# Kernel optimization log

Hardware: AMD Instinct MI355X
Metric: run time of the kernel (lower is better)

## Reference

```python
import jax, jax.numpy as jnp
import numpy as np

D = 1024      # model_dim
H = 2048      # expert hidden_dim
E = 8         # num routed experts
TOP_K = 2
N_SHARED = 1
B, S = 2, 1024


def setup_inputs() -> dict:
    key = jax.random.key(0)
    ks = jax.random.split(key, 12)
    sc = 0.02
    return {
        "hidden": jax.random.normal(ks[0], (B, S, D), jnp.float32),
        # router Linear(D -> E); stored as [in, out]
        "router_w": jax.random.normal(ks[1], (D, E), jnp.float32) * sc,
        "router_b": jnp.zeros((E,), jnp.float32),
        # shared expert (1): Linear(D->H), Linear(H->D)
        "sw1": jax.random.normal(ks[2], (D, H), jnp.float32) * sc,
        "sb1": jnp.zeros((H,), jnp.float32),
        "sw2": jax.random.normal(ks[3], (H, D), jnp.float32) * sc,
        "sb2": jnp.zeros((D,), jnp.float32),
        # routed experts, stacked over E
        "rw1": jax.random.normal(ks[4], (E, D, H), jnp.float32) * sc,
        "rb1": jnp.zeros((E, H), jnp.float32),
        "rw2": jax.random.normal(ks[5], (E, H, D), jnp.float32) * sc,
        "rb2": jnp.zeros((E, D), jnp.float32),
    }


def reference(hidden, router_w, router_b, sw1, sb1, sw2, sb2, rw1, rb1, rw2, rb2):
    b, s, d = hidden.shape
    T = b * s
    flat = hidden.reshape(T, d)                              # [T, D]

    # --- router ---
    router_logits = flat @ router_w + router_b               # [T, E]
    router_probs = jax.nn.softmax(router_logits, axis=-1)
    topk_probs, topk_idx = jax.lax.top_k(router_probs, TOP_K)  # [T, K]

    # per-(token, expert) mixing weight: sum of top-k probs that hit expert e
    weights = jnp.zeros_like(router_probs).at[
        jnp.arange(T)[:, None], topk_idx
    ].add(topk_probs)                                        # [T, E]

    # --- shared expert(s) (1 expert -> mean == itself) ---
    sh = jax.nn.gelu(flat @ sw1 + sb1, approximate=False)    # [T, H]
    shared_out = (sh @ sw2 + sb2) / N_SHARED                 # [T, D]

    # --- routed experts: dense all-expert eval weighted by routing weights ---
    # (identical math to the gather/FFN/index_add loop: weight is 0 for
    #  tokens not routed to expert e)
    h1 = jax.nn.gelu(jnp.einsum('td,edh->teh', flat, rw1) + rb1[None],
                     approximate=False)                      # [T, E, H]
    expert_out = jnp.einsum('teh,ehd->ted', h1, rw2) + rb2[None]  # [T, E, D]
    mixed = jnp.einsum('ted,te->td', expert_out, weights)    # [T, D]

    return (shared_out + mixed).reshape(b, s, d)
```

## Files before the change

kernel.cpp:

```cpp
#include <hip/hip_runtime.h>
#include <hip/hip_bf16.h>

#define T_TOK 2048
#define DDIM  1024
#define HDIM  2048
#define NEXP  8
#define NSEG  9

typedef unsigned short u16;
typedef __attribute__((ext_vector_type(4))) float f32x4;
typedef __attribute__((ext_vector_type(8))) short bf16x8;
typedef __attribute__((ext_vector_type(4))) unsigned short u16x4;

__device__ __forceinline__ u16 f2bf(float x) {
  union { float f; unsigned int u; } v; v.f = x;
  unsigned int r = v.u + 0x7fffu + ((v.u >> 16) & 1u);
  return (u16)(r >> 16);
}
__device__ __forceinline__ float gelu_exact(float x) {
  return 0.5f * x * (1.0f + erff(x * 0.70710678118654752f));
}

__device__ __forceinline__ void gload16(const void* g, void* l) {
  __builtin_amdgcn_global_load_lds(
      (const __attribute__((address_space(1))) unsigned int*)g,
      (__attribute__((address_space(3))) unsigned int*)l, 16, 0, 0);
}

__global__ __launch_bounds__(256) void router_kernel(
    const float* __restrict__ x, const float* __restrict__ rw,
    const float* __restrict__ rb, u16* __restrict__ xb,
    float* __restrict__ weights, int* __restrict__ counts,
    int* __restrict__ lists)
{
  int wv = threadIdx.x >> 6, lane = threadIdx.x & 63;
  int t = blockIdx.x * 4 + wv;
  const float* xrow = x + (size_t)t * DDIM;
  float acc[NEXP];
#pragma unroll
  for (int e = 0; e < NEXP; e++) acc[e] = 0.f;
#pragma unroll
  for (int i = 0; i < 4; i++) {
    int d0 = i * 256 + lane * 4;
    f32x4 xv = *(const f32x4*)(xrow + d0);
    u16x4 pk;
#pragma unroll
    for (int j = 0; j < 4; j++) {
      float xs = xv[j];
      pk[j] = f2bf(xs);
      const float* wr = rw + (size_t)(d0 + j) * NEXP;
#pragma unroll
      for (int e = 0; e < NEXP; e++) acc[e] = fmaf(xs, wr[e], acc[e]);
    }
    *(u16x4*)(xb + (size_t)t * DDIM + d0) = pk;
  }
#pragma unroll
  for (int off = 32; off >= 1; off >>= 1)
#pragma unroll
    for (int e = 0; e < NEXP; e++) acc[e] += __shfl_xor(acc[e], off);

  if (lane == 0) {
    float lg[NEXP], mx = -1e30f;
#pragma unroll
    for (int e = 0; e < NEXP; e++) { lg[e] = acc[e] + rb[e]; mx = fmaxf(mx, lg[e]); }
    float p[NEXP], s = 0.f;
#pragma unroll
    for (int e = 0; e < NEXP; e++) { p[e] = expf(lg[e] - mx); s += p[e]; }
    float inv = 1.0f / s;
#pragma unroll
    for (int e = 0; e < NEXP; e++) p[e] *= inv;
    int i1 = 0;
#pragma unroll
    for (int e = 1; e < NEXP; e++) if (p[e] > p[i1]) i1 = e;
    int i2 = (i1 == 0) ? 1 : 0;
#pragma unroll
    for (int e = 0; e < NEXP; e++) if (e != i1 && p[e] > p[i2]) i2 = e;
#pragma unroll
    for (int e = 0; e < NEXP; e++)
      weights[(size_t)t * NEXP + e] = (e == i1) ? p[i1] : (e == i2) ? p[i2] : 0.f;
    int p1 = atomicAdd(counts + i1, 1); lists[i1 * T_TOK + p1] = t;
    int p2 = atomicAdd(counts + i2, 1); lists[i2 * T_TOK + p2] = t;
    lists[NEXP * T_TOK + t] = t;
  }
}

__global__ void seg_kernel(int* counts, int* segoff, int* ytab, int* nyt) {
  counts[NEXP] = T_TOK;
  int off = 0, n = 0;
  for (int e = 0; e < NSEG; e++) {
    segoff[e] = off;
    int c = counts[e];
    for (int my = 0; my * 128 < c; my++) ytab[n++] = e * 256 + my;
    off += c;
  }
  *nyt = n;
}

__global__ __launch_bounds__(256) void transpose_bf16_kernel(
    const float* __restrict__ rin, const float* __restrict__ sin_,
    u16* __restrict__ rout, u16* __restrict__ sout, int R, int C)
{
  __shared__ float tile[32][33];
  int b = blockIdx.z;
  const float* inb = (b < NEXP) ? rin + (size_t)b * R * C : sin_;
  u16* outb = (b < NEXP) ? rout + (size_t)b * R * C : sout;
  int r0 = blockIdx.y * 32, c0 = blockIdx.x * 32;
  int tx = threadIdx.x & 31, ty = threadIdx.x >> 5;
#pragma unroll
  for (int j = 0; j < 4; j++) {
    int r = ty + j * 8;
    tile[r][tx] = inb[(size_t)(r0 + r) * C + c0 + tx];
  }
  __syncthreads();
#pragma unroll
  for (int j = 0; j < 4; j++) {
    int rr = ty + j * 8;
    outb[(size_t)(c0 + rr) * R + r0 + tx] = f2bf(tile[tx][rr]);
  }
}

__global__ __launch_bounds__(256) void gemm1_kernel(
    const u16* __restrict__ Xb, const u16* __restrict__ rw1t,
    const u16* __restrict__ sw1t, const float* __restrict__ rb1,
    const float* __restrict__ sb1, const int* __restrict__ counts,
    const int* __restrict__ segoff, const int* __restrict__ lists,
    const int* __restrict__ ytab, const int* __restrict__ nyt,
    u16* __restrict__ H1)
{
  __shared__ u16 Alds[128 * 64];
  __shared__ u16 Blds[128 * 64];

  int tid = threadIdx.x, wv = tid >> 6, lane = tid & 63;
  int wm = wv >> 1, wn = wv & 1;
  int col8 = (lane & 7) * 8;

  int ntile = nyt[0] * (HDIM / 128);
  for (int t = blockIdx.x; t < ntile; t += gridDim.x) {
    int yt = t >> 4, nx = t & 15;
    int em = ytab[yt];
    int e = em >> 8, m0 = (em & 255) * 128, n0 = nx * 128;
    int cnt = counts[e];
    const u16* Bt = (e < NEXP) ? (rw1t + (size_t)e * HDIM * DDIM) : sw1t;
    const float* bias = (e < NEXP) ? (rb1 + (size_t)e * HDIM) : sb1;
    const int* list = lists + e * T_TOK;
    int seg = segoff[e];

    size_t asrc[4], bsrc[4];
#pragma unroll
    for (int r = 0; r < 4; r++) {
      int srow = r * 32 + wv * 8 + (lane >> 3);
      int tok = list[min(m0 + srow, cnt - 1)];
      asrc[r] = (size_t)tok * DDIM + col8;
      bsrc[r] = (size_t)(n0 + srow) * DDIM + col8;
    }

    f32x4 acc[4][4];
#pragma unroll
    for (int i = 0; i < 4; i++)
#pragma unroll
      for (int j = 0; j < 4; j++) acc[i][j] = (f32x4){0.f, 0.f, 0.f, 0.f};

    for (int kk = 0; kk < DDIM; kk += 64) {
#pragma unroll
      for (int r = 0; r < 4; r++) {
        gload16(Xb + asrc[r] + kk, Alds + (size_t)(r * 256 + wv * 64 + lane) * 8);
        gload16(Bt + bsrc[r] + kk, Blds + (size_t)(r * 256 + wv * 64 + lane) * 8);
      }
      __syncthreads();
#pragma unroll
      for (int ks = 0; ks < 2; ks++) {
        int kb = ks * 32 + (lane >> 4) * 8;
        bf16x8 af[4], bfr[4];
#pragma unroll
        for (int f = 0; f < 4; f++) {
          af[f]  = *(const bf16x8*)(Alds + (wm * 64 + f * 16 + (lane & 15)) * 64 + kb);
          bfr[f] = *(const bf16x8*)(Blds + (wn * 64 + f * 16 + (lane & 15)) * 64 + kb);
        }
#pragma unroll
        for (int mf = 0; mf < 4; mf++)
#pragma unroll
          for (int nf = 0; nf < 4; nf++)
            acc[mf][nf] = __builtin_amdgcn_mfma_f32_16x16x32_bf16(af[mf], bfr[nf], acc[mf][nf], 0, 0, 0);
      }
      __syncthreads();
    }

#pragma unroll
    for (int nf = 0; nf < 4; nf++) {
      int col = n0 + wn * 64 + nf * 16 + (lane & 15);
      float b = bias[col];
#pragma unroll
      for (int mf = 0; mf < 4; mf++) {
#pragma unroll
        for (int rg = 0; rg < 4; rg++) {
          int mt = wm * 64 + mf * 16 + (lane >> 4) * 4 + rg;
          if (m0 + mt < cnt) {
            float v = acc[mf][nf][rg] + b;
            H1[(size_t)(seg + m0 + mt) * HDIM + col] = f2bf(gelu_exact(v));
          }
        }
      }
    }
  }
}

__global__ __launch_bounds__(256) void gemm2_kernel(
    const u16* __restrict__ H1, const u16* __restrict__ rw2t,
    const u16* __restrict__ sw2t, const float* __restrict__ rb2,
    const float* __restrict__ sb2, const float* __restrict__ weights,
    const int* __restrict__ counts, const int* __restrict__ segoff,
    const int* __restrict__ lists, const int* __restrict__ ytab,
    const int* __restrict__ nyt, float* __restrict__ out)
{
  __shared__ u16 Alds[128 * 64];
  __shared__ u16 Blds[128 * 64];

  int tid = threadIdx.x, wv = tid >> 6, lane = tid & 63;
  int wm = wv >> 1, wn = wv & 1;
  int col8 = (lane & 7) * 8;

  int ntile = nyt[0] * (DDIM / 128);
  for (int t = blockIdx.x; t < ntile; t += gridDim.x) {
    int yt = t >> 3, nx = t & 7;
    int em = ytab[yt];
    int e = em >> 8, m0 = (em & 255) * 128, n0 = nx * 128;
    int cnt = counts[e];
    const u16* Bt = (e < NEXP) ? (rw2t + (size_t)e * DDIM * HDIM) : sw2t;
    const float* bias = (e < NEXP) ? (rb2 + (size_t)e * DDIM) : sb2;
    const int* list = lists + e * T_TOK;
    int seg = segoff[e];

    size_t asrc[4], bsrc[4];
#pragma unroll
    for (int r = 0; r < 4; r++) {
      int srow = r * 32 + wv * 8 + (lane >> 3);
      asrc[r] = (size_t)(seg + min(m0 + srow, cnt - 1)) * HDIM + col8;
      bsrc[r] = (size_t)(n0 + srow) * HDIM + col8;
    }

    f32x4 acc[4][4];
#pragma unroll
    for (int i = 0; i < 4; i++)
#pragma unroll
      for (int j = 0; j < 4; j++) acc[i][j] = (f32x4){0.f, 0.f, 0.f, 0.f};

    for (int kk = 0; kk < HDIM; kk += 64) {
#pragma unroll
      for (int r = 0; r < 4; r++) {
        gload16(H1 + asrc[r] + kk, Alds + (size_t)(r * 256 + wv * 64 + lane) * 8);
        gload16(Bt + bsrc[r] + kk, Blds + (size_t)(r * 256 + wv * 64 + lane) * 8);
      }
      __syncthreads();
#pragma unroll
      for (int ks = 0; ks < 2; ks++) {
        int kb = ks * 32 + (lane >> 4) * 8;
        bf16x8 af[4], bfr[4];
#pragma unroll
        for (int f = 0; f < 4; f++) {
          af[f]  = *(const bf16x8*)(Alds + (wm * 64 + f * 16 + (lane & 15)) * 64 + kb);
          bfr[f] = *(const bf16x8*)(Blds + (wn * 64 + f * 16 + (lane & 15)) * 64 + kb);
        }
#pragma unroll
        for (int mf = 0; mf < 4; mf++)
#pragma unroll
          for (int nf = 0; nf < 4; nf++)
            acc[mf][nf] = __builtin_amdgcn_mfma_f32_16x16x32_bf16(af[mf], bfr[nf], acc[mf][nf], 0, 0, 0);
      }
      __syncthreads();
    }

    float biasv[4];
#pragma unroll
    for (int nf = 0; nf < 4; nf++) biasv[nf] = bias[n0 + wn * 64 + nf * 16 + (lane & 15)];

#pragma unroll
    for (int mf = 0; mf < 4; mf++) {
#pragma unroll
      for (int rg = 0; rg < 4; rg++) {
        int mt = wm * 64 + mf * 16 + (lane >> 4) * 4 + rg;
        int mrow = m0 + mt;
        if (mrow < cnt) {
          int tok = list[mrow];
          float w = (e < NEXP) ? weights[(size_t)tok * NEXP + e] : 1.0f;
          float* orow = out + (size_t)tok * DDIM + n0 + wn * 64 + (lane & 15);
#pragma unroll
          for (int nf = 0; nf < 4; nf++)
            atomicAdd(orow + nf * 16, w * (acc[mf][nf][rg] + biasv[nf]));
        }
      }
    }
  }
}

extern "C" void kernel_launch(void* const* d_in, const int* in_sizes, int n_in,
                              void* d_out, int out_size, void* d_ws, size_t ws_size,
                              hipStream_t stream) {
  (void)in_sizes; (void)n_in; (void)out_size; (void)ws_size;
  const float* hidden   = (const float*)d_in[0];
  const float* router_w = (const float*)d_in[1];
  const float* router_b = (const float*)d_in[2];
  const float* sw1 = (const float*)d_in[3];
  const float* sb1 = (const float*)d_in[4];
  const float* sw2 = (const float*)d_in[5];
  const float* sb2 = (const float*)d_in[6];
  const float* rw1 = (const float*)d_in[7];
  const float* rb1 = (const float*)d_in[8];
  const float* rw2 = (const float*)d_in[9];
  const float* rb2 = (const float*)d_in[10];
  float* out = (float*)d_out;

  char* ws = (char*)d_ws;
  u16* Xb      = (u16*)(ws + 0);
  u16* rw1t    = (u16*)(ws + 4194304);
  u16* rw2t    = (u16*)(ws + 37748736);
  u16* sw1t    = (u16*)(ws + 71303168);
  u16* sw2t    = (u16*)(ws + 75497472);
  u16* H1      = (u16*)(ws + 79691776);
  float* weights = (float*)(ws + 104857600);
  int* counts  = (int*)(ws + 104923136);
  int* segoff  = (int*)(ws + 104923200);
  int* lists   = (int*)(ws + 104923264);
  int* ytab    = (int*)(ws + 104996992);
  int* nyt     = (int*)(ws + 104997632);

  hipMemsetAsync(counts, 0, 64, stream);
  hipMemsetAsync(out, 0, (size_t)T_TOK * DDIM * sizeof(float), stream);

  router_kernel<<<T_TOK / 4, 256, 0, stream>>>(hidden, router_w, router_b, Xb,
                                               weights, counts, lists);
  seg_kernel<<<1, 1, 0, stream>>>(counts, segoff, ytab, nyt);

  transpose_bf16_kernel<<<dim3(HDIM / 32, DDIM / 32, NSEG), 256, 0, stream>>>(
      rw1, sw1, rw1t, sw1t, DDIM, HDIM);
  transpose_bf16_kernel<<<dim3(DDIM / 32, HDIM / 32, NSEG), 256, 0, stream>>>(
      rw2, sw2, rw2t, sw2t, HDIM, DDIM);

  gemm1_kernel<<<1024, 256, 0, stream>>>(
      Xb, rw1t, sw1t, rb1, sb1, counts, segoff, lists, ytab, nyt, H1);
  gemm2_kernel<<<1024, 256, 0, stream>>>(
      H1, rw2t, sw2t, rb2, sb2, weights, counts, segoff, lists, ytab, nyt, out);
}
```

Baseline: 256.1 us.

## Fuse fp32 weight transpose-convert into GEMM loads, split-K gemm2, fast GELU

Drops the separate transpose/bf16 conversion kernels. Each GEMM now reads the fp32 weights directly, converts them to bf16 in registers with a one-step register prefetch, and stores them into XOR-swizzled LDS to avoid bank conflicts. gemm2 splits K into two halves to get more tiles, which doubles the output atomics. The exact erf GELU is replaced with a tanh-style sigmoid approximation, which changes numerics slightly.

```diff
diff --git a/kernel.cpp b/kernel.cpp
--- a/kernel.cpp
+++ b/kernel.cpp
@@ -11,14 +11,16 @@
 typedef __attribute__((ext_vector_type(4))) float f32x4;
 typedef __attribute__((ext_vector_type(8))) short bf16x8;
 typedef __attribute__((ext_vector_type(4))) unsigned short u16x4;
+typedef __attribute__((ext_vector_type(8))) unsigned short u16x8;
 
 __device__ __forceinline__ u16 f2bf(float x) {
   union { float f; unsigned int u; } v; v.f = x;
   unsigned int r = v.u + 0x7fffu + ((v.u >> 16) & 1u);
   return (u16)(r >> 16);
 }
-__device__ __forceinline__ float gelu_exact(float x) {
-  return 0.5f * x * (1.0f + erff(x * 0.70710678118654752f));
+__device__ __forceinline__ float gelu_fast(float x) {
+  float y = x * (1.595769122f + 0.0713548162f * x * x);
+  return x / (1.0f + __expf(-y));
 }
 
 __device__ __forceinline__ void gload16(const void* g, void* l) {
@@ -96,32 +98,10 @@
   *nyt = n;
 }
 
-__global__ __launch_bounds__(256) void transpose_bf16_kernel(
-    const float* __restrict__ rin, const float* __restrict__ sin_,
-    u16* __restrict__ rout, u16* __restrict__ sout, int R, int C)
-{
-  __shared__ float tile[32][33];
-  int b = blockIdx.z;
-  const float* inb = (b < NEXP) ? rin + (size_t)b * R * C : sin_;
-  u16* outb = (b < NEXP) ? rout + (size_t)b * R * C : sout;
-  int r0 = blockIdx.y * 32, c0 = blockIdx.x * 32;
-  int tx = threadIdx.x & 31, ty = threadIdx.x >> 5;
-#pragma unroll
-  for (int j = 0; j < 4; j++) {
-    int r = ty + j * 8;
-    tile[r][tx] = inb[(size_t)(r0 + r) * C + c0 + tx];
-  }
-  __syncthreads();
-#pragma unroll
-  for (int j = 0; j < 4; j++) {
-    int rr = ty + j * 8;
-    outb[(size_t)(c0 + rr) * R + r0 + tx] = f2bf(tile[tx][rr]);
-  }
-}
 
 __global__ __launch_bounds__(256) void gemm1_kernel(
-    const u16* __restrict__ Xb, const u16* __restrict__ rw1t,
-    const u16* __restrict__ sw1t, const float* __restrict__ rb1,
+    const u16* __restrict__ Xb, const float* __restrict__ rw1,
+    const float* __restrict__ sw1, const float* __restrict__ rb1,
     const float* __restrict__ sb1, const int* __restrict__ counts,
     const int* __restrict__ segoff, const int* __restrict__ lists,
     const int* __restrict__ ytab, const int* __restrict__ nyt,
@@ -130,9 +110,27 @@
   __shared__ u16 Alds[128 * 64];
   __shared__ u16 Blds[128 * 64];
 
-  int tid = threadIdx.x, wv = tid >> 6, lane = tid & 63;
-  int wm = wv >> 1, wn = wv & 1;
-  int col8 = (lane & 7) * 8;
+  int tid = threadIdx.x, lane = tid & 63;
+  int wv = tid >> 6, wm = wv >> 1, wn = wv & 1;
+  int kc = lane >> 4, lr = lane & 15;
+
+  int srow[4]; int achk[4];
+#pragma unroll
+  for (int r = 0; r < 4; r++) {
+    srow[r] = r * 32 + wv * 8 + (lane >> 3);
+    achk[r] = ((lane & 7) ^ (srow[r] & 7)) * 8;
+  }
+  int aoff[2][4], boff[2][4];
+#pragma unroll
+  for (int ks = 0; ks < 2; ks++)
+#pragma unroll
+    for (int f = 0; f < 4; f++) {
+      int ra = wm * 64 + f * 16 + lr;
+      int rb_ = wn * 64 + f * 16 + lr;
+      aoff[ks][f] = ra * 64 + (((ks * 4 + kc) ^ (ra & 7)) * 8);
+      boff[ks][f] = rb_ * 64 + (((ks * 4 + kc) ^ (rb_ & 7)) * 8);
+    }
+  int h8 = tid >> 5, bn = (lane & 31) * 4;
 
   int ntile = nyt[0] * (HDIM / 128);
   for (int t = blockIdx.x; t < ntile; t += gridDim.x) {
@@ -140,19 +138,18 @@
     int em = ytab[yt];
     int e = em >> 8, m0 = (em & 255) * 128, n0 = nx * 128;
     int cnt = counts[e];
-    const u16* Bt = (e < NEXP) ? (rw1t + (size_t)e * HDIM * DDIM) : sw1t;
+    const float* Wf = (e < NEXP) ? (rw1 + (size_t)e * DDIM * HDIM) : sw1;
     const float* bias = (e < NEXP) ? (rb1 + (size_t)e * HDIM) : sb1;
     const int* list = lists + e * T_TOK;
     int seg = segoff[e];
 
-    size_t asrc[4], bsrc[4];
+    size_t asrc[4];
 #pragma unroll
     for (int r = 0; r < 4; r++) {
-      int srow = r * 32 + wv * 8 + (lane >> 3);
-      int tok = list[min(m0 + srow, cnt - 1)];
-      asrc[r] = (size_t)tok * DDIM + col8;
-      bsrc[r] = (size_t)(n0 + srow) * DDIM + col8;
-    }
+      int tok = list[min(m0 + srow[r], cnt - 1)];
+      asrc[r] = (size_t)tok * DDIM + achk[r];
+    }
+    const float* Wb = Wf + n0 + bn;
 
     f32x4 acc[4][4];
 #pragma unroll
@@ -160,21 +157,40 @@
 #pragma unroll
       for (int j = 0; j < 4; j++) acc[i][j] = (f32x4){0.f, 0.f, 0.f, 0.f};
 
-    for (int kk = 0; kk < DDIM; kk += 64) {
-#pragma unroll
-      for (int r = 0; r < 4; r++) {
+    f32x4 vb[8];
+    {
+      const float* Wk = Wb + (size_t)(h8 * 8) * HDIM;
+#pragma unroll
+      for (int q = 0; q < 8; q++) vb[q] = *(const f32x4*)(Wk + (size_t)q * HDIM);
+    }
+
+    const int NS = DDIM / 64;
+    for (int s = 0; s < NS; s++) {
+      int kk = s * 64;
+#pragma unroll
+      for (int r = 0; r < 4; r++)
         gload16(Xb + asrc[r] + kk, Alds + (size_t)(r * 256 + wv * 64 + lane) * 8);
-        gload16(Bt + bsrc[r] + kk, Blds + (size_t)(r * 256 + wv * 64 + lane) * 8);
+#pragma unroll
+      for (int j = 0; j < 4; j++) {
+        u16x8 pk;
+#pragma unroll
+        for (int q = 0; q < 8; q++) pk[q] = f2bf(vb[q][j]);
+        int row = bn + j;
+        *(u16x8*)(Blds + (size_t)row * 64 + ((h8 ^ (row & 7)) * 8)) = pk;
       }
       __syncthreads();
+      if (s + 1 < NS) {
+        const float* Wk = Wb + (size_t)((s + 1) * 64 + h8 * 8) * HDIM;
+#pragma unroll
+        for (int q = 0; q < 8; q++) vb[q] = *(const f32x4*)(Wk + (size_t)q * HDIM);
+      }
 #pragma unroll
       for (int ks = 0; ks < 2; ks++) {
-        int kb = ks * 32 + (lane >> 4) * 8;
         bf16x8 af[4], bfr[4];
 #pragma unroll
         for (int f = 0; f < 4; f++) {
-          af[f]  = *(const bf16x8*)(Alds + (wm * 64 + f * 16 + (lane & 15)) * 64 + kb);
-          bfr[f] = *(const bf16x8*)(Blds + (wn * 64 + f * 16 + (lane & 15)) * 64 + kb);
+          af[f]  = *(const bf16x8*)(Alds + aoff[ks][f]);
+          bfr[f] = *(const bf16x8*)(Blds + boff[ks][f]);
         }
 #pragma unroll
         for (int mf = 0; mf < 4; mf++)
@@ -187,16 +203,16 @@
 
 #pragma unroll
     for (int nf = 0; nf < 4; nf++) {
-      int col = n0 + wn * 64 + nf * 16 + (lane & 15);
+      int col = n0 + wn * 64 + nf * 16 + lr;
       float b = bias[col];
 #pragma unroll
       for (int mf = 0; mf < 4; mf++) {
 #pragma unroll
         for (int rg = 0; rg < 4; rg++) {
-          int mt = wm * 64 + mf * 16 + (lane >> 4) * 4 + rg;
+          int mt = wm * 64 + mf * 16 + kc * 4 + rg;
           if (m0 + mt < cnt) {
             float v = acc[mf][nf][rg] + b;
-            H1[(size_t)(seg + m0 + mt) * HDIM + col] = f2bf(gelu_exact(v));
+            H1[(size_t)(seg + m0 + mt) * HDIM + col] = f2bf(gelu_fast(v));
           }
         }
       }
@@ -205,8 +221,8 @@
 }
 
 __global__ __launch_bounds__(256) void gemm2_kernel(
-    const u16* __restrict__ H1, const u16* __restrict__ rw2t,
-    const u16* __restrict__ sw2t, const float* __restrict__ rb2,
+    const u16* __restrict__ H1, const float* __restrict__ rw2,
+    const float* __restrict__ sw2, const float* __restrict__ rb2,
     const float* __restrict__ sb2, const float* __restrict__ weights,
     const int* __restrict__ counts, const int* __restrict__ segoff,
     const int* __restrict__ lists, const int* __restrict__ ytab,
@@ -215,28 +231,45 @@
   __shared__ u16 Alds[128 * 64];
   __shared__ u16 Blds[128 * 64];
 
-  int tid = threadIdx.x, wv = tid >> 6, lane = tid & 63;
-  int wm = wv >> 1, wn = wv & 1;
-  int col8 = (lane & 7) * 8;
-
-  int ntile = nyt[0] * (DDIM / 128);
+  int tid = threadIdx.x, lane = tid & 63;
+  int wv = tid >> 6, wm = wv >> 1, wn = wv & 1;
+  int kc = lane >> 4, lr = lane & 15;
+
+  int srow[4]; int achk[4];
+#pragma unroll
+  for (int r = 0; r < 4; r++) {
+    srow[r] = r * 32 + wv * 8 + (lane >> 3);
+    achk[r] = ((lane & 7) ^ (srow[r] & 7)) * 8;
+  }
+  int aoff[2][4], boff[2][4];
+#pragma unroll
+  for (int ks = 0; ks < 2; ks++)
+#pragma unroll
+    for (int f = 0; f < 4; f++) {
+      int ra = wm * 64 + f * 16 + lr;
+      int rb_ = wn * 64 + f * 16 + lr;
+      aoff[ks][f] = ra * 64 + (((ks * 4 + kc) ^ (ra & 7)) * 8);
+      boff[ks][f] = rb_ * 64 + (((ks * 4 + kc) ^ (rb_ & 7)) * 8);
+    }
+  int h8 = tid >> 5, bn = (lane & 31) * 4;
+
+  int ntile = nyt[0] * (DDIM / 128) * 2;
   for (int t = blockIdx.x; t < ntile; t += gridDim.x) {
-    int yt = t >> 3, nx = t & 7;
+    int kh = t & 1, nx = (t >> 1) & 7, yt = t >> 4;
     int em = ytab[yt];
     int e = em >> 8, m0 = (em & 255) * 128, n0 = nx * 128;
     int cnt = counts[e];
-    const u16* Bt = (e < NEXP) ? (rw2t + (size_t)e * DDIM * HDIM) : sw2t;
+    const float* Wf = (e < NEXP) ? (rw2 + (size_t)e * HDIM * DDIM) : sw2;
     const float* bias = (e < NEXP) ? (rb2 + (size_t)e * DDIM) : sb2;
     const int* list = lists + e * T_TOK;
     int seg = segoff[e];
-
-    size_t asrc[4], bsrc[4];
-#pragma unroll
-    for (int r = 0; r < 4; r++) {
-      int srow = r * 32 + wv * 8 + (lane >> 3);
-      asrc[r] = (size_t)(seg + min(m0 + srow, cnt - 1)) * HDIM + col8;
-      bsrc[r] = (size_t)(n0 + srow) * HDIM + col8;
-    }
+    int k0 = kh * 1024;
+
+    size_t asrc[4];
+#pragma unroll
+    for (int r = 0; r < 4; r++)
+      asrc[r] = (size_t)(seg + min(m0 + srow[r], cnt - 1)) * HDIM + k0 + achk[r];
+    const float* Wb = Wf + (size_t)k0 * DDIM + n0 + bn;
 
     f32x4 acc[4][4];
 #pragma unroll
@@ -244,21 +277,40 @@
 #pragma unroll
       for (int j = 0; j < 4; j++) acc[i][j] = (f32x4){0.f, 0.f, 0.f, 0.f};
 
-    for (int kk = 0; kk < HDIM; kk += 64) {
-#pragma unroll
-      for (int r = 0; r < 4; r++) {
+    f32x4 vb[8];
+    {
+      const float* Wk = Wb + (size_t)(h8 * 8) * DDIM;
+#pragma unroll
+      for (int q = 0; q < 8; q++) vb[q] = *(const f32x4*)(Wk + (size_t)q * DDIM);
+    }
+
+    const int NS = 1024 / 64;
+    for (int s = 0; s < NS; s++) {
+      int kk = s * 64;
+#pragma unroll
+      for (int r = 0; r < 4; r++)
         gload16(H1 + asrc[r] + kk, Alds + (size_t)(r * 256 + wv * 64 + lane) * 8);
-        gload16(Bt + bsrc[r] + kk, Blds + (size_t)(r * 256 + wv * 64 + lane) * 8);
+#pragma unroll
+      for (int j = 0; j < 4; j++) {
+        u16x8 pk;
+#pragma unroll
+        for (int q = 0; q < 8; q++) pk[q] = f2bf(vb[q][j]);
+        int row = bn + j;
+        *(u16x8*)(Blds + (size_t)row * 64 + ((h8 ^ (row & 7)) * 8)) = pk;
       }
       __syncthreads();
+      if (s + 1 < NS) {
+        const float* Wk = Wb + (size_t)((s + 1) * 64 + h8 * 8) * DDIM;
+#pragma unroll
+        for (int q = 0; q < 8; q++) vb[q] = *(const f32x4*)(Wk + (size_t)q * DDIM);
+      }
 #pragma unroll
       for (int ks = 0; ks < 2; ks++) {
-        int kb = ks * 32 + (lane >> 4) * 8;
         bf16x8 af[4], bfr[4];
 #pragma unroll
         for (int f = 0; f < 4; f++) {
-          af[f]  = *(const bf16x8*)(Alds + (wm * 64 + f * 16 + (lane & 15)) * 64 + kb);
-          bfr[f] = *(const bf16x8*)(Blds + (wn * 64 + f * 16 + (lane & 15)) * 64 + kb);
+          af[f]  = *(const bf16x8*)(Alds + aoff[ks][f]);
+          bfr[f] = *(const bf16x8*)(Blds + boff[ks][f]);
         }
 #pragma unroll
         for (int mf = 0; mf < 4; mf++)
@@ -271,18 +323,19 @@
 
     float biasv[4];
 #pragma unroll
-    for (int nf = 0; nf < 4; nf++) biasv[nf] = bias[n0 + wn * 64 + nf * 16 + (lane & 15)];
+    for (int nf = 0; nf < 4; nf++)
+      biasv[nf] = (kh == 0) ? bias[n0 + wn * 64 + nf * 16 + lr] : 0.f;
 
 #pragma unroll
     for (int mf = 0; mf < 4; mf++) {
 #pragma unroll
       for (int rg = 0; rg < 4; rg++) {
-        int mt = wm * 64 + mf * 16 + (lane >> 4) * 4 + rg;
+        int mt = wm * 64 + mf * 16 + kc * 4 + rg;
         int mrow = m0 + mt;
         if (mrow < cnt) {
           int tok = list[mrow];
           float w = (e < NEXP) ? weights[(size_t)tok * NEXP + e] : 1.0f;
-          float* orow = out + (size_t)tok * DDIM + n0 + wn * 64 + (lane & 15);
+          float* orow = out + (size_t)tok * DDIM + n0 + wn * 64 + lr;
 #pragma unroll
           for (int nf = 0; nf < 4; nf++)
             atomicAdd(orow + nf * 16, w * (acc[mf][nf][rg] + biasv[nf]));
@@ -311,17 +364,13 @@
 
   char* ws = (char*)d_ws;
   u16* Xb      = (u16*)(ws + 0);
-  u16* rw1t    = (u16*)(ws + 4194304);
-  u16* rw2t    = (u16*)(ws + 37748736);
-  u16* sw1t    = (u16*)(ws + 71303168);
-  u16* sw2t    = (u16*)(ws + 75497472);
-  u16* H1      = (u16*)(ws + 79691776);
-  float* weights = (float*)(ws + 104857600);
-  int* counts  = (int*)(ws + 104923136);
-  int* segoff  = (int*)(ws + 104923200);
-  int* lists   = (int*)(ws + 104923264);
-  int* ytab    = (int*)(ws + 104996992);
-  int* nyt     = (int*)(ws + 104997632);
+  u16* H1      = (u16*)(ws + 4194304);
+  float* weights = (float*)(ws + 29360128);
+  int* counts  = (int*)(ws + 29425664);
+  int* segoff  = (int*)(ws + 29425728);
+  int* lists   = (int*)(ws + 29425792);
+  int* ytab    = (int*)(ws + 29499520);
+  int* nyt     = (int*)(ws + 29500160);
 
   hipMemsetAsync(counts, 0, 64, stream);
   hipMemsetAsync(out, 0, (size_t)T_TOK * DDIM * sizeof(float), stream);
@@ -330,13 +379,8 @@
                                                weights, counts, lists);
   seg_kernel<<<1, 1, 0, stream>>>(counts, segoff, ytab, nyt);
 
-  transpose_bf16_kernel<<<dim3(HDIM / 32, DDIM / 32, NSEG), 256, 0, stream>>>(
-      rw1, sw1, rw1t, sw1t, DDIM, HDIM);
-  transpose_bf16_kernel<<<dim3(DDIM / 32, HDIM / 32, NSEG), 256, 0, stream>>>(
-      rw2, sw2, rw2t, sw2t, HDIM, DDIM);
-
   gemm1_kernel<<<1024, 256, 0, stream>>>(
-      Xb, rw1t, sw1t, rb1, sb1, counts, segoff, lists, ytab, nyt, H1);
+      Xb, rw1, sw1, rb1, sb1, counts, segoff, lists, ytab, nyt, H1);
   gemm2_kernel<<<1024, 256, 0, stream>>>(
-      H1, rw2t, sw2t, rb2, sb2, weights, counts, segoff, lists, ytab, nyt, out);
-}
+      H1, rw2, sw2, rb2, sb2, weights, counts, segoff, lists, ytab, nyt, out);
+}
```

Measured after the change: 285.6 us. 11.5% more time.
